# Kernel optimization log

Measured on AMD Instinct MI355X. Metric: run time of the kernel, lower is better.

## Reference

```python
import jax, jax.numpy as jnp
import numpy as np

H, DH = 8, 64  # num_heads, head_dim


def setup_inputs() -> dict:
    key = jax.random.key(0)
    ks = jax.random.split(key, 7)
    m, nq, nkv, d = 4, 2048, 2048, 512
    return {
        "xq": jax.random.normal(ks[0], (m, nq, d), jnp.float32),
        "xk": jax.random.normal(ks[1], (m, nkv, d), jnp.float32),
        "xv": jax.random.normal(ks[2], (m, nkv, d), jnp.float32),
        "Wq": jax.random.normal(ks[3], (d, H * DH), jnp.float32) * 0.02,
        "Wk": jax.random.normal(ks[4], (d, H * DH), jnp.float32) * 0.02,
        "Wv": jax.random.normal(ks[5], (d, H * DH), jnp.float32) * 0.02,
        "Wo": jax.random.normal(ks[6], (H * DH, d), jnp.float32) * 0.02,
        "bo": jnp.zeros((d,), jnp.float32),
    }


def _split_heads(t):
    # [b, n, h*d] -> [b, h, n, d]
    b, n, _ = t.shape
    return t.reshape(b, n, H, DH).transpose(0, 2, 1, 3)


def reference(xq, xk, xv, Wq, Wk, Wv, Wo, bo):
    scale = DH ** -0.5
    q = _split_heads(xq @ Wq)   # [b,h,nq,dh]
    k = _split_heads(xk @ Wk)   # [b,h,nkv,dh]
    v = _split_heads(xv @ Wv)   # [b,h,nkv,dh]
    dots = jnp.einsum("bhqd,bhkd->bhqk", q, k) * scale  # [b,h,nq,nkv]
    # diagonal attention term: query attends to its own (k,v) projection
    xq_k = _split_heads(xq @ Wk)
    xq_v = _split_heads(xq @ Wv)
    diag = jnp.sum(q * xq_k, axis=-1, keepdims=True) * scale  # [b,h,nq,1]
    dots = jnp.concatenate([dots, diag], axis=-1)  # [b,h,nq,nkv+1]
    attn = jax.nn.softmax(dots, axis=-1)
    out = jnp.einsum("bhqk,bhkd->bhqd", attn[..., :-1], v) + attn[..., -1:] * xq_v
    b, _, nq, _ = out.shape
    out = out.transpose(0, 2, 1, 3).reshape(b, nq, H * DH)  # merge heads
    return out @ Wo + bo
```

## Files before the change

### kernel.cpp

```cpp
#include <hip/hip_runtime.h>

#define LOG2E 1.44269504088896f
#define CS (0.125f * LOG2E)

typedef __bf16 bf16x8 __attribute__((ext_vector_type(8)));
typedef float f32x4 __attribute__((ext_vector_type(4)));
typedef float f32x16 __attribute__((ext_vector_type(16)));
typedef unsigned short u16x8 __attribute__((ext_vector_type(8)));

#if __has_builtin(__builtin_amdgcn_exp2f)
#define fexp2(x) __builtin_amdgcn_exp2f(x)
#else
extern "C" __device__ float __ocml_native_exp2_f32(float);
#define fexp2(x) __ocml_native_exp2_f32(x)
#endif

__device__ __forceinline__ unsigned short f2bf(float f) {
  union { float f; unsigned int u; } v{f};
  unsigned int r = v.u + 0x7fffu + ((v.u >> 16) & 1u);
  return (unsigned short)(r >> 16);
}
__device__ __forceinline__ float bf2f(unsigned short u) {
  union { unsigned int u; float f; } v; v.u = ((unsigned int)u) << 16; return v.f;
}
__device__ __forceinline__ unsigned int pkr(float a, float b) {
  unsigned int ua = __builtin_bit_cast(unsigned int, a) + 0x8000u;
  unsigned int ub = __builtin_bit_cast(unsigned int, b) + 0x8000u;
  return __builtin_amdgcn_perm(ub, ua, 0x07060302);
}

#define PLSWAP(x, y) asm("v_permlane32_swap_b32 %0, %1" : "+v"(x), "+v"(y))

typedef __attribute__((address_space(3))) unsigned int lds32_t;
typedef const __attribute__((address_space(1))) unsigned int glb32_t;
__device__ __forceinline__ void gld16(const unsigned short* g, unsigned short* l) {
  __builtin_amdgcn_global_load_lds((glb32_t*)(unsigned long long)g,
                                   (lds32_t*)(unsigned int)(unsigned long long)l,
                                   16, 0, 0);
}

__global__ __launch_bounds__(256) void conv_all(
    const float* __restrict__ xq, const float* __restrict__ xk, const float* __restrict__ xv,
    const float* __restrict__ Wq, const float* __restrict__ Wk,
    const float* __restrict__ Wv, const float* __restrict__ Wo,
    unsigned short* __restrict__ oxq, unsigned short* __restrict__ oxk, unsigned short* __restrict__ oxv,
    unsigned short* __restrict__ oWq, unsigned short* __restrict__ oWk,
    unsigned short* __restrict__ oWv, unsigned short* __restrict__ oWo) {
  __shared__ unsigned short T[64 * 65];
  const int blk = blockIdx.x;
  if (blk < 12288) {
    const int N4 = (8192 * 512) / 4;
    int idx = blk * 256 + threadIdx.x;
    const float* src; unsigned short* dst; int i;
    if (idx < N4)          { src = xq; dst = oxq; i = idx; }
    else if (idx < 2 * N4) { src = xk; dst = oxk; i = idx - N4; }
    else                   { src = xv; dst = oxv; i = idx - 2 * N4; }
    float4 v = ((const float4*)src)[i];
    ushort4 o; o.x = f2bf(v.x); o.y = f2bf(v.y); o.z = f2bf(v.z); o.w = f2bf(v.w);
    ((ushort4*)dst)[i] = o;
  } else {
    const int wblk = blk - 12288;
    const int wsel = wblk >> 6;
    const int tile = wblk & 63;
    const int tk = (tile >> 3) * 64, tn = (tile & 7) * 64;
    const float* src = (wsel == 0) ? Wq : (wsel == 1) ? Wk : (wsel == 2) ? Wv : Wo;
    unsigned short* dst = (wsel == 0) ? oWq : (wsel == 1) ? oWk : (wsel == 2) ? oWv : oWo;
    const float scale = (wsel == 0) ? CS : 1.0f;
    const int rr = threadIdx.x >> 4;
    const int cc = (threadIdx.x & 15) * 4;
#pragma unroll
    for (int i = 0; i < 4; i++) {
      int row = rr + i * 16;
      float4 v = *(const float4*)&src[(size_t)(tk + row) * 512 + tn + cc];
      T[(cc + 0) * 65 + row] = f2bf(v.x * scale);
      T[(cc + 1) * 65 + row] = f2bf(v.y * scale);
      T[(cc + 2) * 65 + row] = f2bf(v.z * scale);
      T[(cc + 3) * 65 + row] = f2bf(v.w * scale);
    }
    __syncthreads();
#pragma unroll
    for (int i = 0; i < 4; i++) {
      int n = rr + i * 16;
      ushort4 o;
      o.x = T[n * 65 + cc + 0]; o.y = T[n * 65 + cc + 1];
      o.z = T[n * 65 + cc + 2]; o.w = T[n * 65 + cc + 3];
      *(ushort4*)&dst[(size_t)(tn + n) * 512 + tk + cc] = o;
    }
  }
}

__device__ __forceinline__ void gemm_tile(
    const unsigned short* __restrict__ A, const unsigned short* __restrict__ Bt,
    int rowBlk, int colBlk, unsigned short* As, unsigned short* Bs, f32x4 (&acc)[4][4]) {
  const int t = threadIdx.x;
  const int lane = t & 63, c = lane & 15, g = lane >> 4;
  const int w = t >> 6;
  const int wm = w & 1, wn = w >> 1;
#pragma unroll
  for (int i = 0; i < 4; i++)
#pragma unroll
    for (int j = 0; j < 4; j++)
#pragma unroll
      for (int r = 0; r < 4; r++) acc[i][j][r] = 0.f;

  const int sr = t >> 2, sch = t & 3;
#define STAGE_PROJ(kkk, buf)                                                     \
  do {                                                                           \
    unsigned short* Ad = As + (buf) * (128 * 32);                                \
    unsigned short* Bd = Bs + (buf) * (128 * 32);                                \
    gld16(&A[(size_t)(rowBlk + sr) * 512 + (kkk) + sch * 8], &Ad[t * 8]);        \
    gld16(&Bt[(size_t)(colBlk + sr) * 512 + (kkk) + sch * 8], &Bd[t * 8]);       \
    gld16(&A[(size_t)(rowBlk + sr + 64) * 512 + (kkk) + sch * 8],                \
          &Ad[(t + 256) * 8]);                                                   \
    gld16(&Bt[(size_t)(colBlk + sr + 64) * 512 + (kkk) + sch * 8],               \
          &Bd[(t + 256) * 8]);                                                   \
  } while (0)

  STAGE_PROJ(0, 0);
  __syncthreads();

  for (int kt = 0; kt < 16; kt++) {
    if (kt < 15) STAGE_PROJ((kt + 1) * 32, (kt + 1) & 1);
    const unsigned short* Ac = As + (kt & 1) * (128 * 32);
    const unsigned short* Bc = Bs + (kt & 1) * (128 * 32);
    bf16x8 af[4], bfr[4];
#pragma unroll
    for (int i = 0; i < 4; i++)
      af[i] = __builtin_bit_cast(bf16x8, *(const u16x8*)&Ac[(wm * 64 + i * 16 + c) * 32 + g * 8]);
#pragma unroll
    for (int j = 0; j < 4; j++)
      bfr[j] = __builtin_bit_cast(bf16x8, *(const u16x8*)&Bc[(wn * 64 + j * 16 + c) * 32 + g * 8]);
#pragma unroll
    for (int i = 0; i < 4; i++)
#pragma unroll
      for (int j = 0; j < 4; j++)
        acc[i][j] = __builtin_amdgcn_mfma_f32_16x16x32_bf16(af[i], bfr[j], acc[i][j], 0, 0, 0);
    if (kt < 15) __syncthreads();
  }
#undef STAGE_PROJ
}

__global__ __launch_bounds__(256) void proj_all(
    const unsigned short* __restrict__ xq, const unsigned short* __restrict__ xk,
    const unsigned short* __restrict__ xv,
    const unsigned short* __restrict__ Wq, const unsigned short* __restrict__ Wk,
    const unsigned short* __restrict__ Wv,
    unsigned short* __restrict__ Qo, unsigned short* __restrict__ XKo,
    unsigned short* __restrict__ XVo, unsigned short* __restrict__ Ko,
    unsigned short* __restrict__ Vto) {
  __shared__ unsigned short As[2 * 128 * 32];
  __shared__ unsigned short Bs[2 * 128 * 32];
  const int rowBlk = blockIdx.x * 128;
  const int y = blockIdx.y;
  const unsigned short* A; const unsigned short* Bt; int colBlk; int mode;
  unsigned short* out;
  if (y < 12) {
    int wsel = y >> 2;
    A = xq; colBlk = (y & 3) * 128; mode = 0;
    Bt = (wsel == 0) ? Wq : (wsel == 1) ? Wk : Wv;
    out = (wsel == 0) ? Qo : (wsel == 1) ? XKo : XVo;
  } else if (y < 16) {
    A = xk; Bt = Wk; out = Ko; colBlk = (y - 12) * 128; mode = 0;
  } else {
    A = xv; Bt = Wv; out = Vto; colBlk = (y - 16) * 128; mode = 1;
  }
  f32x4 acc[4][4];
  gemm_tile(A, Bt, rowBlk, colBlk, As, Bs, acc);
  const int t = threadIdx.x;
  const int w = t >> 6, lane = t & 63, c = lane & 15, g = lane >> 4;
  const int wm = w & 1, wn = w >> 1;
  if (mode == 0) {
#pragma unroll
    for (int i = 0; i < 4; i++)
#pragma unroll
      for (int j = 0; j < 4; j++)
#pragma unroll
        for (int r = 0; r < 4; r++) {
          int row = rowBlk + wm * 64 + i * 16 + g * 4 + r;
          int col = colBlk + wn * 64 + j * 16 + c;
          out[(size_t)row * 512 + col] = f2bf(acc[i][j][r]);
        }
  } else {
#pragma unroll
    for (int i = 0; i < 4; i++) {
      int tok0 = rowBlk + wm * 64 + i * 16 + g * 4;
      int bb = tok0 >> 11, n0 = tok0 & 2047;
#pragma unroll
      for (int j = 0; j < 4; j++) {
        int col = colBlk + wn * 64 + j * 16 + c;
        int hh = col >> 6, dh = col & 63;
        ushort4 o;
        o.x = f2bf(acc[i][j][0]); o.y = f2bf(acc[i][j][1]);
        o.z = f2bf(acc[i][j][2]); o.w = f2bf(acc[i][j][3]);
        *(ushort4*)&out[((size_t)(bb * 8 + hh) * 64 + dh) * 2048 + n0] = o;
      }
    }
  }
}

__global__ __launch_bounds__(256) void gemm_out(
    const unsigned short* __restrict__ A, const unsigned short* __restrict__ Bt,
    float* __restrict__ out, const float* __restrict__ bias) {
  __shared__ unsigned short As[2 * 128 * 32];
  __shared__ unsigned short Bs[2 * 64 * 32];
  const int rowBlk = blockIdx.x * 128;
  const int colBlk = blockIdx.y * 64;
  const int t = threadIdx.x;
  const int lane = t & 63, c = lane & 15, g = lane >> 4;
  const int w = t >> 6;
  const int wm = w & 1, wn = w >> 1;
  f32x4 acc[4][2];
#pragma unroll
  for (int i = 0; i < 4; i++)
#pragma unroll
    for (int j = 0; j < 2; j++)
#pragma unroll
      for (int r = 0; r < 4; r++) acc[i][j][r] = 0.f;

  const int sr = t >> 2, sch = t & 3;
#define STAGE_OUT(kkk, buf)                                                      \
  do {                                                                           \
    unsigned short* Ad = As + (buf) * (128 * 32);                                \
    unsigned short* Bd = Bs + (buf) * (64 * 32);                                 \
    gld16(&A[(size_t)(rowBlk + sr) * 512 + (kkk) + sch * 8], &Ad[t * 8]);        \
    gld16(&A[(size_t)(rowBlk + sr + 64) * 512 + (kkk) + sch * 8],                \
          &Ad[(t + 256) * 8]);                                                   \
    gld16(&Bt[(size_t)(colBlk + sr) * 512 + (kkk) + sch * 8], &Bd[t * 8]);       \
  } while (0)

  STAGE_OUT(0, 0);
  __syncthreads();

  for (int kt = 0; kt < 16; kt++) {
    if (kt < 15) STAGE_OUT((kt + 1) * 32, (kt + 1) & 1);
    const unsigned short* Ac = As + (kt & 1) * (128 * 32);
    const unsigned short* Bc = Bs + (kt & 1) * (64 * 32);
    bf16x8 af[4], bfr[2];
#pragma unroll
    for (int i = 0; i < 4; i++)
      af[i] = __builtin_bit_cast(bf16x8, *(const u16x8*)&Ac[(wm * 64 + i * 16 + c) * 32 + g * 8]);
#pragma unroll
    for (int j = 0; j < 2; j++)
      bfr[j] = __builtin_bit_cast(bf16x8, *(const u16x8*)&Bc[(wn * 32 + j * 16 + c) * 32 + g * 8]);
#pragma unroll
    for (int i = 0; i < 4; i++)
#pragma unroll
      for (int j = 0; j < 2; j++)
        acc[i][j] = __builtin_amdgcn_mfma_f32_16x16x32_bf16(af[i], bfr[j], acc[i][j], 0, 0, 0);
    if (kt < 15) __syncthreads();
  }
#undef STAGE_OUT
#pragma unroll
  for (int i = 0; i < 4; i++)
#pragma unroll
    for (int j = 0; j < 2; j++)
#pragma unroll
      for (int r = 0; r < 4; r++) {
        int row = rowBlk + wm * 64 + i * 16 + g * 4 + r;
        int col = colBlk + wn * 32 + j * 16 + c;
        out[(size_t)row * 512 + col] = acc[i][j][r] + bias[col];
      }
}

__global__ __launch_bounds__(512, 2) void attn_kernel(
    const unsigned short* __restrict__ Q, const unsigned short* __restrict__ K,
    const unsigned short* __restrict__ Vt, const unsigned short* __restrict__ XK,
    const unsigned short* __restrict__ XV, unsigned short* __restrict__ O) {
  __shared__ unsigned short Ks[2][64 * 64];
  __shared__ unsigned short Vs[2][64 * 64];
  __shared__ float Fin[8][2][32];
  const int t = threadIdx.x;
  const int w = t >> 6, lane = t & 63;
  const int rowA = lane & 31, hi = lane >> 5, l7 = lane & 7;
  const int id = blockIdx.x;
  const int h = id & 7, qt = (id >> 3) & 7, b = id >> 6;
  const size_t hb = (size_t)b * (2048 * 512) + h * 64;
  const size_t vhb = (size_t)(b * 8 + h) * 64 * 2048;
  const int qb0 = qt * 256 + w * 32;

  const int sr = t >> 3, sch = t & 7;
  const int ssl = (sch ^ (sr & 7)) * 8;
  const size_t kgoff = hb + (size_t)sr * 512 + ssl;
  const size_t vgoff = vhb + (size_t)sr * 2048 + ssl;

  bf16x8 qf[4];
#pragma unroll
  for (int d = 0; d < 4; d++)
    qf[d] = __builtin_bit_cast(bf16x8,
        *(const u16x8*)&Q[hb + (size_t)(qb0 + rowA) * 512 + d * 16 + hi * 8]);

  f32x16 accO[2];
#pragma unroll
  for (int n = 0; n < 2; n++)
#pragma unroll
    for (int r = 0; r < 16; r++) accO[n][r] = 0.f;
  float lq = 0.f;

  gld16(&K[kgoff], &Ks[0][t * 8]);
  gld16(&Vt[vgoff], &Vs[0][t * 8]);
  __syncthreads();

  for (int kt = 0; kt < 32; kt++) {
    const int cb = kt & 1;
    if (kt < 31) {
      gld16(&K[kgoff + (size_t)(kt + 1) * (64 * 512)], &Ks[cb ^ 1][t * 8]);
      gld16(&Vt[vgoff + (size_t)(kt + 1) * 64], &Vs[cb ^ 1][t * 8]);
    }
    const unsigned short* Kc = &Ks[cb][0];
    const unsigned short* Vc = &Vs[cb][0];

    f32x16 s0, s1;
#pragma unroll
    for (int r = 0; r < 16; r++) { s0[r] = 0.f; s1[r] = 0.f; }
    __builtin_amdgcn_s_setprio(1);
#pragma unroll
    for (int d = 0; d < 4; d++) {
      bf16x8 k0 = __builtin_bit_cast(bf16x8,
          *(const u16x8*)&Kc[rowA * 64 + (((d * 2 + hi) ^ l7) * 8)]);
      s0 = __builtin_amdgcn_mfma_f32_32x32x16_bf16(k0, qf[d], s0, 0, 0, 0);
    }
#pragma unroll
    for (int d = 0; d < 4; d++) {
      bf16x8 k1 = __builtin_bit_cast(bf16x8,
          *(const u16x8*)&Kc[(32 + rowA) * 64 + (((d * 2 + hi) ^ l7) * 8)]);
      s1 = __builtin_amdgcn_mfma_f32_32x32x16_bf16(k1, qf[d], s1, 0, 0, 0);
    }
    __builtin_amdgcn_s_setprio(0);

    float sum = 0.f;
#pragma unroll
    for (int r = 0; r < 16; r++) { s0[r] = fexp2(s0[r]); sum += s0[r]; }
#pragma unroll
    for (int r = 0; r < 16; r++) { s1[r] = fexp2(s1[r]); sum += s1[r]; }
    lq += sum;

#define PVSUB(P, T2)                                                            \
  {                                                                             \
    unsigned int x0 = pkr(P[0], P[1]),   y0 = pkr(P[4], P[5]);                  \
    unsigned int x1 = pkr(P[2], P[3]),   y1 = pkr(P[6], P[7]);                  \
    unsigned int x2 = pkr(P[8], P[9]),   y2 = pkr(P[12], P[13]);                \
    unsigned int x3 = pkr(P[10], P[11]), y3 = pkr(P[14], P[15]);                \
    PLSWAP(x0, y0); PLSWAP(x1, y1); PLSWAP(x2, y2); PLSWAP(x3, y3);             \
    uint4 w0 = {x0, x1, y0, y1};                                                \
    uint4 w1 = {x2, x3, y2, y3};                                                \
    bf16x8 pa0 = __builtin_bit_cast(bf16x8, w0);                                \
    bf16x8 pa1 = __builtin_bit_cast(bf16x8, w1);                                \
    _Pragma("unroll")                                                           \
    for (int n = 0; n < 2; n++) {                                               \
      bf16x8 v0 = __builtin_bit_cast(bf16x8,                                    \
          *(const u16x8*)&Vc[(n * 32 + rowA) * 64 + ((((T2) * 4 + hi) ^ l7) * 8)]); \
      bf16x8 v1 = __builtin_bit_cast(bf16x8,                                    \
          *(const u16x8*)&Vc[(n * 32 + rowA) * 64 + ((((T2) * 4 + 2 + hi) ^ l7) * 8)]); \
      accO[n] = __builtin_amdgcn_mfma_f32_32x32x16_bf16(pa0, v0, accO[n], 0, 0, 0); \
      accO[n] = __builtin_amdgcn_mfma_f32_32x32x16_bf16(pa1, v1, accO[n], 0, 0, 0); \
    }                                                                           \
  }
    __builtin_amdgcn_s_setprio(1);
    PVSUB(s0, 0);
    PVSUB(s1, 1);
    __builtin_amdgcn_s_setprio(0);
#undef PVSUB

    if (kt < 31) __syncthreads();
  }

  lq += __shfl_xor(lq, 32);

  float part = 0.f;
  {
    const size_t base = hb + (size_t)(qb0 + rowA) * 512 + hi * 32;
#pragma unroll
    for (int ii = 0; ii < 4; ii++) {
      u16x8 q8 = *(const u16x8*)&Q[base + ii * 8];
      u16x8 x8 = *(const u16x8*)&XK[base + ii * 8];
#pragma unroll
      for (int e = 0; e < 8; e++) part += bf2f(q8[e]) * bf2f(x8[e]);
    }
  }
  part += __shfl_xor(part, 32);
  float pd = fexp2(part);
  float inv = 1.f / (lq + pd);
  if (lane < 32) {
    Fin[w][0][rowA] = inv;
    Fin[w][1][rowA] = pd * inv;
  }
  __builtin_amdgcn_s_waitcnt(0);

  f32x4 inva[4], pia[4];
#pragma unroll
  for (int rq = 0; rq < 4; rq++) {
    inva[rq] = *(const f32x4*)&Fin[w][0][rq * 8 + hi * 4];
    pia[rq]  = *(const f32x4*)&Fin[w][1][rq * 8 + hi * 4];
  }
#pragma unroll
  for (int n = 0; n < 2; n++)
#pragma unroll
    for (int reg = 0; reg < 16; reg++) {
      const int rq = reg >> 2, r = reg & 3;
      const int q = rq * 8 + hi * 4 + r;
      const int qrow = qb0 + q;
      float xv = bf2f(XV[hb + (size_t)qrow * 512 + n * 32 + rowA]);
      float val = accO[n][reg] * inva[rq][r] + pia[rq][r] * xv;
      O[((size_t)(b * 2048 + qrow)) * 512 + h * 64 + n * 32 + rowA] = f2bf(val);
    }
}

extern "C" void kernel_launch(void* const* d_in, const int* in_sizes, int n_in,
                              void* d_out, int out_size, void* d_ws, size_t ws_size,
                              hipStream_t stream) {
  const float* xq = (const float*)d_in[0];
  const float* xk = (const float*)d_in[1];
  const float* xv = (const float*)d_in[2];
  const float* Wq = (const float*)d_in[3];
  const float* Wk = (const float*)d_in[4];
  const float* Wv = (const float*)d_in[5];
  const float* Wo = (const float*)d_in[6];
  const float* bo = (const float*)d_in[7];

  unsigned short* ws = (unsigned short*)d_ws;
  const size_t MD = 8192ull * 512;
  const size_t WD = 512ull * 512;
  unsigned short* xq_b = ws;
  unsigned short* xk_b = xq_b + MD;
  unsigned short* xv_b = xk_b + MD;
  unsigned short* Wq_t = xv_b + MD;
  unsigned short* Wk_t = Wq_t + WD;
  unsigned short* Wv_t = Wk_t + WD;
  unsigned short* Wo_t = Wv_t + WD;
  unsigned short* Qb  = Wo_t + WD;
  unsigned short* Kb  = Qb + MD;
  unsigned short* Vtb = Kb + MD;
  unsigned short* XKb = Vtb + MD;
  unsigned short* XVb = XKb + MD;
  unsigned short* Ob  = XVb + MD;

  conv_all<<<dim3(12544), 256, 0, stream>>>(xq, xk, xv, Wq, Wk, Wv, Wo,
                                            xq_b, xk_b, xv_b, Wq_t, Wk_t, Wv_t, Wo_t);
  proj_all<<<dim3(64, 20), 256, 0, stream>>>(xq_b, xk_b, xv_b, Wq_t, Wk_t, Wv_t,
                                             Qb, XKb, XVb, Kb, Vtb);
  attn_kernel<<<dim3(256), 512, 0, stream>>>(Qb, Kb, Vtb, XKb, XVb, Ob);
  gemm_out<<<dim3(64, 8), 256, 0, stream>>>(Ob, Wo_t, (float*)d_out, bo);
}
```

Before: 201.2 us.

## Split attention KV range across two warp groups to double block count

Each attention block now covers 128 query rows instead of 256. Its 8 waves form two groups that each handle half of the 2048 KV positions, and the two partial accumulators and row sums are merged through shared memory at the end. This doubles the grid from 256 to 512 blocks so the GPU's compute units are better filled. The cost is twice the shared memory for K/V double buffers, a reduction step at the end, and K/V tiles being loaded by twice as many blocks.

```diff
diff --git a/kernel.cpp b/kernel.cpp
--- a/kernel.cpp
+++ b/kernel.cpp
@@ -266,17 +266,18 @@
     const unsigned short* __restrict__ Q, const unsigned short* __restrict__ K,
     const unsigned short* __restrict__ Vt, const unsigned short* __restrict__ XK,
     const unsigned short* __restrict__ XV, unsigned short* __restrict__ O) {
-  __shared__ unsigned short Ks[2][64 * 64];
-  __shared__ unsigned short Vs[2][64 * 64];
-  __shared__ float Fin[8][2][32];
+  __shared__ unsigned short Ks[2][2][64 * 64];
+  __shared__ unsigned short Vs[2][2][64 * 64];
+  __shared__ float Fin[4][2][32];
   const int t = threadIdx.x;
   const int w = t >> 6, lane = t & 63;
+  const int w01 = w & 3, wk = w >> 2;
   const int rowA = lane & 31, hi = lane >> 5, l7 = lane & 7;
   const int id = blockIdx.x;
-  const int h = id & 7, qt = (id >> 3) & 7, b = id >> 6;
+  const int h = id & 7, qt = (id >> 3) & 15, b = id >> 7;
   const size_t hb = (size_t)b * (2048 * 512) + h * 64;
   const size_t vhb = (size_t)(b * 8 + h) * 64 * 2048;
-  const int qb0 = qt * 256 + w * 32;
+  const int qb0 = qt * 128 + w01 * 32;
 
   const int sr = t >> 3, sch = t & 7;
   const int ssl = (sch ^ (sr & 7)) * 8;
@@ -296,18 +297,22 @@
     for (int r = 0; r < 16; r++) accO[n][r] = 0.f;
   float lq = 0.f;
 
-  gld16(&K[kgoff], &Ks[0][t * 8]);
-  gld16(&Vt[vgoff], &Vs[0][t * 8]);
+  gld16(&K[kgoff], &Ks[0][0][t * 8]);
+  gld16(&K[kgoff + (size_t)16 * (64 * 512)], &Ks[1][0][t * 8]);
+  gld16(&Vt[vgoff], &Vs[0][0][t * 8]);
+  gld16(&Vt[vgoff + 16 * 64], &Vs[1][0][t * 8]);
   __syncthreads();
 
-  for (int kt = 0; kt < 32; kt++) {
+  for (int kt = 0; kt < 16; kt++) {
     const int cb = kt & 1;
-    if (kt < 31) {
-      gld16(&K[kgoff + (size_t)(kt + 1) * (64 * 512)], &Ks[cb ^ 1][t * 8]);
-      gld16(&Vt[vgoff + (size_t)(kt + 1) * 64], &Vs[cb ^ 1][t * 8]);
-    }
-    const unsigned short* Kc = &Ks[cb][0];
-    const unsigned short* Vc = &Vs[cb][0];
+    if (kt < 15) {
+      gld16(&K[kgoff + (size_t)(kt + 1) * (64 * 512)], &Ks[0][cb ^ 1][t * 8]);
+      gld16(&K[kgoff + (size_t)(kt + 17) * (64 * 512)], &Ks[1][cb ^ 1][t * 8]);
+      gld16(&Vt[vgoff + (size_t)(kt + 1) * 64], &Vs[0][cb ^ 1][t * 8]);
+      gld16(&Vt[vgoff + (size_t)(kt + 17) * 64], &Vs[1][cb ^ 1][t * 8]);
+    }
+    const unsigned short* Kc = &Ks[wk][cb][0];
+    const unsigned short* Vc = &Vs[wk][cb][0];
 
     f32x16 s0, s1;
 #pragma unroll
@@ -361,7 +366,28 @@
     __builtin_amdgcn_s_setprio(0);
 #undef PVSUB
 
-    if (kt < 31) __syncthreads();
+    if (kt < 15) __syncthreads();
+  }
+
+  __syncthreads();
+
+  {
+    float* MB = (w01 < 2) ? (float*)&Ks[0][0][0] : (float*)&Vs[0][0][0];
+    const int mbase = ((w01 & 1) * 64 + lane) * 33;
+    if (wk == 1) {
+#pragma unroll
+      for (int n = 0; n < 2; n++)
+#pragma unroll
+        for (int reg = 0; reg < 16; reg++) MB[mbase + n * 16 + reg] = accO[n][reg];
+      MB[mbase + 32] = lq;
+    }
+    __syncthreads();
+    if (wk == 1) return;
+#pragma unroll
+    for (int n = 0; n < 2; n++)
+#pragma unroll
+      for (int reg = 0; reg < 16; reg++) accO[n][reg] += MB[mbase + n * 16 + reg];
+    lq += MB[mbase + 32];
   }
 
   lq += __shfl_xor(lq, 32);
@@ -381,16 +407,16 @@
   float pd = fexp2(part);
   float inv = 1.f / (lq + pd);
   if (lane < 32) {
-    Fin[w][0][rowA] = inv;
-    Fin[w][1][rowA] = pd * inv;
+    Fin[w01][0][rowA] = inv;
+    Fin[w01][1][rowA] = pd * inv;
   }
   __builtin_amdgcn_s_waitcnt(0);
 
   f32x4 inva[4], pia[4];
 #pragma unroll
   for (int rq = 0; rq < 4; rq++) {
-    inva[rq] = *(const f32x4*)&Fin[w][0][rq * 8 + hi * 4];
-    pia[rq]  = *(const f32x4*)&Fin[w][1][rq * 8 + hi * 4];
+    inva[rq] = *(const f32x4*)&Fin[w01][0][rq * 8 + hi * 4];
+    pia[rq]  = *(const f32x4*)&Fin[w01][1][rq * 8 + hi * 4];
   }
 #pragma unroll
   for (int n = 0; n < 2; n++)
@@ -438,6 +464,6 @@
                                             xq_b, xk_b, xv_b, Wq_t, Wk_t, Wv_t, Wo_t);
   proj_all<<<dim3(64, 20), 256, 0, stream>>>(xq_b, xk_b, xv_b, Wq_t, Wk_t, Wv_t,
                                              Qb, XKb, XVb, Kb, Vtb);
-  attn_kernel<<<dim3(256), 512, 0, stream>>>(Qb, Kb, Vtb, XKb, XVb, Ob);
+  attn_kernel<<<dim3(512), 512, 0, stream>>>(Qb, Kb, Vtb, XKb, XVb, Ob);
   gemm_out<<<dim3(64, 8), 256, 0, stream>>>(Ob, Wo_t, (float*)d_out, bo);
 }
```

After: 202.0 us. No clear change (+0.4%).
